# Kernel optimization log

Measured on AMD Instinct MI355X. Metric: run time of the kernel, lower is better.

Reference implementation:

```python
import jax, jax.numpy as jnp
import numpy as np

BS, C_IN, L = 64, 64, 4096
C_OUT, KS, K, RATIO = 128, 7, 4, 4
HIDDEN = C_IN // RATIO
PAD, TEMP = 3, 30.0


def setup_inputs() -> dict:
    key = jax.random.key(0)
    k1, k2, k3, k4, k5 = jax.random.split(key, 5)
    x = jax.random.normal(k1, (BS, C_IN, L), dtype=jnp.float32)
    # attention 1x1 convs stored as matmul matrices
    w_attn1 = jax.random.normal(k2, (HIDDEN, C_IN), dtype=jnp.float32) * (2.0 / C_IN) ** 0.5
    w_attn2 = jax.random.normal(k3, (K, HIDDEN), dtype=jnp.float32) * (2.0 / HIDDEN) ** 0.5
    # K-bank conv weights [K, out, in, ks] and biases [K, out]
    weight = jax.random.normal(k4, (K, C_OUT, C_IN, KS), dtype=jnp.float32) * 0.05
    bias = jax.random.normal(k5, (K, C_OUT), dtype=jnp.float32) * 0.05
    return {"x": x, "w_attn1": w_attn1, "w_attn2": w_attn2, "weight": weight, "bias": bias}


def reference(x, w_attn1, w_attn2, weight, bias):
    # Attention1d: global avg pool -> 1x1 conv -> relu -> 1x1 conv -> softmax(./T)
    pooled = jnp.mean(x, axis=-1)                      # [bs, C_in]
    h = jax.nn.relu(pooled @ w_attn1.T)                # [bs, hidden]
    logits = h @ w_attn2.T                             # [bs, K]
    att = jax.nn.softmax(logits / TEMP, axis=-1)       # [bs, K]

    # softmax-weighted aggregation of the K weight banks -> per-sample kernels
    agg_w = jnp.einsum('bk,koif->boif', att, weight)   # [bs, out, in, ks]
    agg_b = att @ bias                                 # [bs, out]

    # per-sample conv1d (the grouped-conv trick), vectorized with vmap
    def conv_one(xi, wi):
        # xi: [C_in, L], wi: [out, in, ks]
        return jax.lax.conv_general_dilated(
            xi[None], wi, window_strides=(1,), padding=[(PAD, PAD)],
            dimension_numbers=('NCH', 'OIH', 'NCH'))[0]  # [out, L]

    out = jax.vmap(conv_one)(x, agg_w) + agg_b[:, :, None]  # [bs, out, L]
    return out
```

## Files before the change

### kernel.cpp

```cpp
#include <hip/hip_runtime.h>

typedef __bf16 bf16;
typedef __bf16 bf16x8 __attribute__((ext_vector_type(8)));
typedef __bf16 bf16x2 __attribute__((ext_vector_type(2)));
typedef float f32x4 __attribute__((ext_vector_type(4)));

#define BS 64
#define CI 64
#define LEN 4096
#define CO 128
#define KS 7
#define NK 4
#define HID 16
#define TEMP 30.0f

#define KTOT 448
#define WROW 456
#define WBAT (CO * WROW)
#define XROW 72
#define XC 134
#define LTILE 128
#define TPB 8

__global__ void pool_kernel(const float* __restrict__ x, float* __restrict__ pooled) {
    int bc = blockIdx.x;
    const float4* xp = (const float4*)(x + (size_t)bc * LEN);
    int t = threadIdx.x;
    float s = 0.f;
#pragma unroll
    for (int j = 0; j < 4; ++j) {
        float4 v = xp[t + 256 * j];
        s += (v.x + v.y) + (v.z + v.w);
    }
#pragma unroll
    for (int off = 32; off > 0; off >>= 1) s += __shfl_down(s, off, 64);
    __shared__ float red[4];
    if ((t & 63) == 0) red[t >> 6] = s;
    __syncthreads();
    if (t == 0) pooled[bc] = (red[0] + red[1] + red[2] + red[3]) * (1.0f / LEN);
}

__global__ void aggw_kernel(const float* __restrict__ pooled,
                            const float* __restrict__ w1,
                            const float* __restrict__ w2,
                            const float* __restrict__ weight,
                            float* __restrict__ att_g,
                            bf16* __restrict__ wagg) {
    int o = blockIdx.x >> 1;
    int bh = blockIdx.x & 1;
    int t = threadIdx.x;
    __shared__ float p[32 * 64];
    __shared__ float hsh[32 * 16];
    __shared__ float att_s[32][4];
    __shared__ float lw[4 * KTOT];

    const float* wo = weight + (size_t)o * KTOT;
    for (int idx = t; idx < 4 * KTOT; idx += 256) {
        int bank = idx / KTOT;
        int r = idx - bank * KTOT;
        lw[idx] = wo[(size_t)bank * (CO * KTOT) + r];
    }
    for (int idx = t; idx < 32 * 64; idx += 256) p[idx] = pooled[bh * 2048 + idx];
    __syncthreads();

    {
        int bb = t >> 3, h2 = (t & 7) * 2;
#pragma unroll
        for (int u = 0; u < 2; ++u) {
            int hh = h2 + u;
            float s = 0.f;
            for (int i = 0; i < 64; ++i) s += p[bb * 64 + i] * w1[hh * 64 + i];
            hsh[bb * 16 + hh] = fmaxf(s, 0.f);
        }
    }
    __syncthreads();
    if (t < 32) {
        float lg[NK], m = -1e30f;
#pragma unroll
        for (int k = 0; k < NK; ++k) {
            float s = 0.f;
            for (int j = 0; j < HID; ++j) s += hsh[t * 16 + j] * w2[k * HID + j];
            lg[k] = s * (1.0f / TEMP);
            m = fmaxf(m, lg[k]);
        }
        float e[NK], tot = 0.f;
#pragma unroll
        for (int k = 0; k < NK; ++k) { e[k] = expf(lg[k] - m); tot += e[k]; }
        float inv = 1.0f / tot;
#pragma unroll
        for (int k = 0; k < NK; ++k) {
            att_s[t][k] = e[k] * inv;
            if (blockIdx.x < 2) att_g[(bh * 32 + t) * NK + k] = e[k] * inv;
        }
    }
    __syncthreads();

    if (t < 224) {
        float w8[8];
#pragma unroll
        for (int j = 0; j < 2; ++j) {
            int kout = 2 * t + j;
            int i = kout & 63, f = kout >> 6;
#pragma unroll
            for (int bank = 0; bank < 4; ++bank)
                w8[j * 4 + bank] = lw[bank * KTOT + i * KS + f];
        }
        for (int bb = 0; bb < 32; ++bb) {
            int b = bh * 32 + bb;
            float a0 = att_s[bb][0], a1 = att_s[bb][1];
            float a2 = att_s[bb][2], a3 = att_s[bb][3];
            float v0 = a0 * w8[0] + a1 * w8[1] + a2 * w8[2] + a3 * w8[3];
            float v1 = a0 * w8[4] + a1 * w8[5] + a2 * w8[6] + a3 * w8[7];
            bf16x2 pk; pk[0] = (bf16)v0; pk[1] = (bf16)v1;
            *(bf16x2*)(wagg + (size_t)b * WBAT + o * WROW + 2 * t) = pk;
        }
    }
}

struct XStage { float4 m[8]; float e1, e2; };

__global__ __launch_bounds__(256, 2) void conv_kernel(
    const float* __restrict__ x,
    const bf16* __restrict__ wagg,
    const float* __restrict__ att_g,
    const float* __restrict__ bias,
    float* __restrict__ out) {
    __shared__ __align__(16) bf16 lds_x[2][XC * XROW];
    __shared__ float aggb_l[CO];

    int nwg = gridDim.x;
    int bid = blockIdx.x;
    int logical = (bid & 7) * (nwg >> 3) + (bid >> 3);
    int b = logical >> 3;
    int rem = logical & 7;
    int oh = rem >> 2, lsp = rem & 3;

    int t = threadIdx.x;
    int lane = t & 63, wid = t >> 6;
    int ln = lane & 15, g = lane >> 4;
    int wm = wid >> 1, wn = wid & 1;

    if (t < CO) {
        float a0 = att_g[b * NK + 0], a1 = att_g[b * NK + 1];
        float a2 = att_g[b * NK + 2], a3 = att_g[b * NK + 3];
        aggb_l[t] = a0 * bias[0 * CO + t] + a1 * bias[1 * CO + t] +
                    a2 * bias[2 * CO + t] + a3 * bias[3 * CO + t];
    }

    const bf16* wgb = wagg + (size_t)b * WBAT
                    + (size_t)(oh * 64 + wm * 32 + ln) * WROW + g * 8;
    bf16x8 av[2][14];
#pragma unroll
    for (int mf = 0; mf < 2; ++mf)
#pragma unroll
        for (int kk = 0; kk < 14; ++kk)
            av[mf][kk] = *(const bf16x8*)(wgb + mf * 16 * WROW + kk * 32);

    int l0base = lsp * (LTILE * TPB);
    int si = t >> 2, sf = t & 3;
    const float* xb = x + (size_t)b * CI * LEN;

    auto load_x = [&](int l0, XStage& s) {
#pragma unroll
        for (int j = 0; j < 8; ++j) {
            int c4 = sf + 4 * j;
            s.m[j] = *(const float4*)(xb + (size_t)si * LEN + l0 + 4 * c4);
        }
        int i1 = t / 6, s1 = t - i1 * 6;
        int c1 = (s1 < 3) ? s1 : (128 + s1);
        int gl1 = l0 - 3 + c1;
        s.e1 = (gl1 >= 0 && gl1 < LEN) ? xb[(size_t)i1 * LEN + gl1] : 0.f;
        s.e2 = 0.f;
        if (t < 128) {
            int e2 = 256 + t, i2 = e2 / 6, s2 = e2 - i2 * 6;
            int c2 = (s2 < 3) ? s2 : (128 + s2);
            int gl2 = l0 - 3 + c2;
            s.e2 = (gl2 >= 0 && gl2 < LEN) ? xb[(size_t)i2 * LEN + gl2] : 0.f;
        }
    };
    auto write_x = [&](int buf, const XStage& s) {
        bf16* lb = lds_x[buf];
#pragma unroll
        for (int j = 0; j < 8; ++j) {
            int c4 = sf + 4 * j;
#pragma unroll
            for (int dl = 0; dl < 4; ++dl) {
                float v = (&s.m[j].x)[dl];
                lb[(4 * c4 + 3 + dl) * XROW + si] = (bf16)v;
            }
        }
        int i1 = t / 6, s1 = t - i1 * 6;
        int c1 = (s1 < 3) ? s1 : (128 + s1);
        lb[c1 * XROW + i1] = (bf16)s.e1;
        if (t < 128) {
            int e2 = 256 + t, i2 = e2 / 6, s2 = e2 - i2 * 6;
            int c2 = (s2 < 3) ? s2 : (128 + s2);
            lb[c2 * XROW + i2] = (bf16)s.e2;
        }
    };

    XStage s0;
    load_x(l0base, s0);
    write_x(0, s0);
    __syncthreads();

    float bias_r[2][4];
    int orow_off[2][4];
#pragma unroll
    for (int mf = 0; mf < 2; ++mf)
#pragma unroll
        for (int r = 0; r < 4; ++r) {
            int o = oh * 64 + wm * 32 + mf * 16 + g * 4 + r;
            bias_r[mf][r] = aggb_l[o];
            orow_off[mf][r] = (b * CO + o) * LEN;
        }

    for (int tl = 0; tl < TPB; ++tl) {
        int l0 = l0base + tl * LTILE;
        XStage sn;
        if (tl + 1 < TPB) load_x(l0 + LTILE, sn);

        f32x4 acc[2][4];
#pragma unroll
        for (int mf = 0; mf < 2; ++mf)
#pragma unroll
            for (int nf = 0; nf < 4; ++nf)
                acc[mf][nf] = (f32x4){0.f, 0.f, 0.f, 0.f};

        const bf16* bp = lds_x[tl & 1] + (wn * 64 + ln) * XROW + g * 8;

#pragma unroll
        for (int kk = 0; kk < 14; ++kk) {
            int boff = (kk >> 1) * XROW + (kk & 1) * 32;
            bf16x8 bv[4];
#pragma unroll
            for (int nf = 0; nf < 4; ++nf)
                bv[nf] = *(const bf16x8*)(bp + nf * 16 * XROW + boff);
#pragma unroll
            for (int mf = 0; mf < 2; ++mf)
#pragma unroll
                for (int nf = 0; nf < 4; ++nf)
                    acc[mf][nf] = __builtin_amdgcn_mfma_f32_16x16x32_bf16(
                        av[mf][kk], bv[nf], acc[mf][nf], 0, 0, 0);
        }

        if (tl + 1 < TPB) {
            write_x((tl + 1) & 1, sn);
            __syncthreads();
        }

#pragma unroll
        for (int mf = 0; mf < 2; ++mf)
#pragma unroll
            for (int nf = 0; nf < 4; ++nf) {
                int l = l0 + wn * 64 + nf * 16 + ln;
#pragma unroll
                for (int r = 0; r < 4; ++r)
                    out[(size_t)orow_off[mf][r] + l] = acc[mf][nf][r] + bias_r[mf][r];
            }
    }
}

extern "C" void kernel_launch(void* const* d_in, const int* in_sizes, int n_in,
                              void* d_out, int out_size, void* d_ws, size_t ws_size,
                              hipStream_t stream) {
    const float* x  = (const float*)d_in[0];
    const float* w1 = (const float*)d_in[1];
    const float* w2 = (const float*)d_in[2];
    const float* wt = (const float*)d_in[3];
    const float* bs = (const float*)d_in[4];
    float* out = (float*)d_out;

    bf16* wagg = (bf16*)d_ws;
    float* pooled = (float*)((char*)d_ws + (size_t)BS * WBAT * 2);
    float* att_g  = pooled + BS * CI;

    pool_kernel<<<BS * CI, 256, 0, stream>>>(x, pooled);
    aggw_kernel<<<CO * 2, 256, 0, stream>>>(pooled, w1, w2, wt, att_g, wagg);
    conv_kernel<<<BS * 8, 256, 0, stream>>>(x, wagg, att_g, bs, out);
}
```

Baseline: 66.59 us.

## Pretranspose x to swizzled padded bf16 and stage conv tiles via direct global-to-LDS loads

A new transpose kernel replaces the pooling kernel. It converts x once into a length-major, zero-padded, XOR-swizzled bf16 buffer and also writes partial channel sums for the attention pooling. The conv kernel then fills its double-buffered LDS tiles with global_load_lds 16-byte copies instead of loading fp32 registers, converting and scattering. This removes the per-tile conversion and halo handling from the conv inner loop and halves the bytes the conv reads for x. In exchange it adds an extra write and read of a bf16 copy of x through the workspace.

```diff
diff --git a/kernel.cpp b/kernel.cpp
--- a/kernel.cpp
+++ b/kernel.cpp
@@ -17,30 +17,71 @@
 #define KTOT 448
 #define WROW 456
 #define WBAT (CO * WROW)
-#define XROW 72
-#define XC 134
 #define LTILE 128
 #define TPB 8
-
-__global__ void pool_kernel(const float* __restrict__ x, float* __restrict__ pooled) {
-    int bc = blockIdx.x;
-    const float4* xp = (const float4*)(x + (size_t)bc * LEN);
+#define XB_ROWS 4112
+#define XB_ELE (XB_ROWS * 64)
+
+__device__ __forceinline__ void gl_lds16(const void* g, void* l) {
+    auto gp = reinterpret_cast<const __attribute__((address_space(1))) unsigned int*>(
+        reinterpret_cast<unsigned long long>(g));
+    auto lp = reinterpret_cast<__attribute__((address_space(3))) unsigned int*>(
+        reinterpret_cast<unsigned long long>(l));
+    __builtin_amdgcn_global_load_lds(gp, lp, 16, 0, 0);
+}
+
+__global__ __launch_bounds__(256) void trans_kernel(const float* __restrict__ x,
+                                                    bf16* __restrict__ xbf,
+                                                    float* __restrict__ part) {
+    int bid = blockIdx.x;
+    int b = bid >> 3, lt = bid & 7;
     int t = threadIdx.x;
-    float s = 0.f;
-#pragma unroll
-    for (int j = 0; j < 4; ++j) {
-        float4 v = xp[t + 256 * j];
-        s += (v.x + v.y) + (v.z + v.w);
-    }
-#pragma unroll
-    for (int off = 32; off > 0; off >>= 1) s += __shfl_down(s, off, 64);
-    __shared__ float red[4];
-    if ((t & 63) == 0) red[t >> 6] = s;
-    __syncthreads();
-    if (t == 0) pooled[bc] = (red[0] + red[1] + red[2] + red[3]) * (1.0f / LEN);
-}
-
-__global__ void aggw_kernel(const float* __restrict__ pooled,
+    int si = t >> 2, sf = t & 3;
+    __shared__ __align__(16) bf16 lds_t[128 * 72];
+    __shared__ float lds_red[64 * 4];
+
+    const float* xb = x + (size_t)b * CI * LEN;
+    bf16* xo = xbf + (size_t)b * XB_ELE;
+    float psum = 0.f;
+
+    for (int st = 0; st < 4; ++st) {
+        int ls = lt * 512 + st * 128;
+        float4 v[8];
+#pragma unroll
+        for (int j = 0; j < 8; ++j)
+            v[j] = *(const float4*)(xb + (size_t)si * LEN + ls + 4 * (sf + 4 * j));
+#pragma unroll
+        for (int j = 0; j < 8; ++j) {
+            psum += (v[j].x + v[j].y) + (v[j].z + v[j].w);
+#pragma unroll
+            for (int e = 0; e < 4; ++e)
+                lds_t[(4 * (sf + 4 * j) + e) * 72 + si] = (bf16)((&v[j].x)[e]);
+        }
+        __syncthreads();
+        int row = t >> 4, l16 = t & 15;
+#pragma unroll
+        for (int pass = 0; pass < 8; ++pass) {
+            int r = pass * 16 + row;
+            int gl = ls + r + 8;
+            uint2 d = *(const uint2*)(lds_t + r * 72 + l16 * 4);
+            int c = l16 >> 1;
+            int sw = c ^ (gl & 7);
+            *(uint2*)((char*)xo + (size_t)gl * 128 + sw * 16 + (l16 & 1) * 8) = d;
+        }
+        __syncthreads();
+    }
+
+    lds_red[si * 4 + sf] = psum;
+    __syncthreads();
+    if (t < 64)
+        part[((size_t)b * 8 + lt) * 64 + t] =
+            lds_red[t * 4] + lds_red[t * 4 + 1] + lds_red[t * 4 + 2] + lds_red[t * 4 + 3];
+
+    if (lt == 0 && t < 128) *(uint2*)((char*)xo + t * 8) = make_uint2(0u, 0u);
+    if (lt == 7 && t < 128) *(uint2*)((char*)xo + (size_t)4104 * 128 + t * 8) = make_uint2(0u, 0u);
+}
+
+__global__ void aggw_kernel(const float* __restrict__ part,
                             const float* __restrict__ w1,
                             const float* __restrict__ w2,
                             const float* __restrict__ weight,
@@ -60,7 +101,14 @@
         int r = idx - bank * KTOT;
         lw[idx] = wo[(size_t)bank * (CO * KTOT) + r];
     }
-    for (int idx = t; idx < 32 * 64; idx += 256) p[idx] = pooled[bh * 2048 + idx];
+    for (int idx = t; idx < 32 * 64; idx += 256) {
+        int bb = idx >> 6, i = idx & 63;
+        const float* pp = part + ((size_t)(bh * 32 + bb) * 8) * 64 + i;
+        float s = 0.f;
+#pragma unroll
+        for (int j = 0; j < 8; ++j) s += pp[j * 64];
+        p[idx] = s * (1.0f / LEN);
+    }
     __syncthreads();
 
     {
@@ -117,15 +165,13 @@
     }
 }
 
-struct XStage { float4 m[8]; float e1, e2; };
-
 __global__ __launch_bounds__(256, 2) void conv_kernel(
-    const float* __restrict__ x,
+    const bf16* __restrict__ xbf,
     const bf16* __restrict__ wagg,
     const float* __restrict__ att_g,
     const float* __restrict__ bias,
     float* __restrict__ out) {
-    __shared__ __align__(16) bf16 lds_x[2][XC * XROW];
+    __shared__ __align__(1024) bf16 lds_x[2][144 * 64];
     __shared__ float aggb_l[CO];
 
     int nwg = gridDim.x;
@@ -157,51 +203,16 @@
             av[mf][kk] = *(const bf16x8*)(wgb + mf * 16 * WROW + kk * 32);
 
     int l0base = lsp * (LTILE * TPB);
-    int si = t >> 2, sf = t & 3;
-    const float* xb = x + (size_t)b * CI * LEN;
-
-    auto load_x = [&](int l0, XStage& s) {
-#pragma unroll
-        for (int j = 0; j < 8; ++j) {
-            int c4 = sf + 4 * j;
-            s.m[j] = *(const float4*)(xb + (size_t)si * LEN + l0 + 4 * c4);
-        }
-        int i1 = t / 6, s1 = t - i1 * 6;
-        int c1 = (s1 < 3) ? s1 : (128 + s1);
-        int gl1 = l0 - 3 + c1;
-        s.e1 = (gl1 >= 0 && gl1 < LEN) ? xb[(size_t)i1 * LEN + gl1] : 0.f;
-        s.e2 = 0.f;
-        if (t < 128) {
-            int e2 = 256 + t, i2 = e2 / 6, s2 = e2 - i2 * 6;
-            int c2 = (s2 < 3) ? s2 : (128 + s2);
-            int gl2 = l0 - 3 + c2;
-            s.e2 = (gl2 >= 0 && gl2 < LEN) ? xb[(size_t)i2 * LEN + gl2] : 0.f;
-        }
+    const bf16* xb = xbf + (size_t)b * XB_ELE;
+
+    auto stage = [&](int buf, int l0) {
+        const char* src = (const char*)xb + (size_t)l0 * 128 + lane * 16;
+        char* dst = (char*)lds_x[buf];
+        for (int c = wid; c < 18; c += 4)
+            gl_lds16(src + c * 1024, dst + c * 1024);
     };
-    auto write_x = [&](int buf, const XStage& s) {
-        bf16* lb = lds_x[buf];
-#pragma unroll
-        for (int j = 0; j < 8; ++j) {
-            int c4 = sf + 4 * j;
-#pragma unroll
-            for (int dl = 0; dl < 4; ++dl) {
-                float v = (&s.m[j].x)[dl];
-                lb[(4 * c4 + 3 + dl) * XROW + si] = (bf16)v;
-            }
-        }
-        int i1 = t / 6, s1 = t - i1 * 6;
-        int c1 = (s1 < 3) ? s1 : (128 + s1);
-        lb[c1 * XROW + i1] = (bf16)s.e1;
-        if (t < 128) {
-            int e2 = 256 + t, i2 = e2 / 6, s2 = e2 - i2 * 6;
-            int c2 = (s2 < 3) ? s2 : (128 + s2);
-            lb[c2 * XROW + i2] = (bf16)s.e2;
-        }
-    };
-
-    XStage s0;
-    load_x(l0base, s0);
-    write_x(0, s0);
+
+    stage(0, l0base);
     __syncthreads();
 
     float bias_r[2][4];
@@ -215,10 +226,11 @@
             orow_off[mf][r] = (b * CO + o) * LEN;
         }
 
+    int prow = wn * 64 + ln + 5;
+
     for (int tl = 0; tl < TPB; ++tl) {
         int l0 = l0base + tl * LTILE;
-        XStage sn;
-        if (tl + 1 < TPB) load_x(l0 + LTILE, sn);
+        if (tl + 1 < TPB) stage((tl + 1) & 1, l0 + LTILE);
 
         f32x4 acc[2][4];
 #pragma unroll
@@ -227,15 +239,17 @@
             for (int nf = 0; nf < 4; ++nf)
                 acc[mf][nf] = (f32x4){0.f, 0.f, 0.f, 0.f};
 
-        const bf16* bp = lds_x[tl & 1] + (wn * 64 + ln) * XROW + g * 8;
+        const char* lb = (const char*)lds_x[tl & 1];
 
 #pragma unroll
         for (int kk = 0; kk < 14; ++kk) {
-            int boff = (kk >> 1) * XROW + (kk & 1) * 32;
+            int f = kk >> 1;
+            int key = (prow + f) & 7;
+            int swz = (((kk & 1) * 4 + g) ^ key) * 16;
             bf16x8 bv[4];
 #pragma unroll
             for (int nf = 0; nf < 4; ++nf)
-                bv[nf] = *(const bf16x8*)(bp + nf * 16 * XROW + boff);
+                bv[nf] = *(const bf16x8*)(lb + (prow + nf * 16 + f) * 128 + swz);
 #pragma unroll
             for (int mf = 0; mf < 2; ++mf)
 #pragma unroll
@@ -244,10 +258,7 @@
                         av[mf][kk], bv[nf], acc[mf][nf], 0, 0, 0);
         }
 
-        if (tl + 1 < TPB) {
-            write_x((tl + 1) & 1, sn);
-            __syncthreads();
-        }
+        if (tl + 1 < TPB) __syncthreads();
 
 #pragma unroll
         for (int mf = 0; mf < 2; ++mf)
@@ -271,11 +282,12 @@
     const float* bs = (const float*)d_in[4];
     float* out = (float*)d_out;
 
-    bf16* wagg = (bf16*)d_ws;
-    float* pooled = (float*)((char*)d_ws + (size_t)BS * WBAT * 2);
-    float* att_g  = pooled + BS * CI;
-
-    pool_kernel<<<BS * CI, 256, 0, stream>>>(x, pooled);
-    aggw_kernel<<<CO * 2, 256, 0, stream>>>(pooled, w1, w2, wt, att_g, wagg);
-    conv_kernel<<<BS * 8, 256, 0, stream>>>(x, wagg, att_g, bs, out);
-}
+    bf16* xbf    = (bf16*)d_ws;
+    bf16* wagg   = (bf16*)((char*)d_ws + (size_t)BS * XB_ELE * 2);
+    float* part  = (float*)((char*)wagg + (size_t)BS * WBAT * 2);
+    float* att_g = part + BS * 8 * 64;
+
+    trans_kernel<<<BS * 8, 256, 0, stream>>>(x, xbf, part);
+    aggw_kernel<<<CO * 2, 256, 0, stream>>>(part, w1, w2, wt, att_g, wagg);
+    conv_kernel<<<BS * 8, 256, 0, stream>>>(xbf, wagg, att_g, bs, out);
+}
```

New measurement: 66.06 us. About the same (-0.8%).
